# Optimization experiments

Hardware: AMD Instinct MI355X
Metric: run time of the kernel (lower is better)

## Reference

```python
import jax, jax.numpy as jnp
import numpy as np

B, C, H, V = 16384, 5, 256, 512
NUM_ITER = 2


def setup_inputs() -> dict:
    key = jax.random.key(0)
    k1, k2, k3, k4 = jax.random.split(key, 4)
    # v0: one-hot categorical visible units, shape [B, C, V, 1]
    idx = jax.random.randint(k1, (B, V), 0, C)
    v0 = jax.nn.one_hot(idx, C, axis=1, dtype=jnp.float32)[..., None]
    W = 0.01 * jax.random.normal(k2, (C, H, V), dtype=jnp.float32)
    b = 0.01 * jax.random.normal(k3, (C, V, 1), dtype=jnp.float32)
    c = 0.01 * jax.random.normal(k4, (H, 1), dtype=jnp.float32)
    return {"v0": v0, "W": W, "b": b, "c": c, "num_sampling_iter": NUM_ITER}


def reference(v0, W, b, c, num_sampling_iter):
    key = jax.random.key(42)
    b2 = b[..., 0]   # [C, V]
    c1 = c[:, 0]     # [H]
    v = v0[..., 0]   # [B, C, V]

    def sample_h(k, v):
        # p(h=1|v) = sigmoid(sum_c W[c] @ v[:,c] + c)
        p = jax.nn.sigmoid(jnp.einsum('chv,bcv->bh', W, v) + c1)  # [B, H]
        return jax.random.bernoulli(k, p).astype(v.dtype)

    def sample_v(k, h):
        # logits over categories per visible unit: W[c].T @ h + b[c]
        logits = jnp.einsum('chv,bh->bcv', W, h) + b2  # [B, C, V]
        idx = jax.random.categorical(k, logits, axis=1)  # [B, V]
        return jax.nn.one_hot(idx, C, axis=1, dtype=h.dtype)  # [B, C, V]

    keys = jax.random.split(key, 2 * num_sampling_iter + 1)
    h = sample_h(keys[0], v)
    h_given_v0 = h
    for i in range(num_sampling_iter):  # small fixed iteration count
        v = sample_v(keys[2 * i + 1], h)
        h = sample_h(keys[2 * i + 2], v)
    return (v[..., None], h[..., None], h_given_v0[..., None])
```

## Files before the change

### kernel.cpp

```cpp
#include <hip/hip_runtime.h>
#include <cstdint>
#include <cstddef>


#define B_DIM 16384
#define C_DIM 5
#define H_DIM 256
#define V_DIM 512

struct TFOut { uint32_t a, b; };

typedef float f32x2 __attribute__((ext_vector_type(2)));
typedef float f32x4 __attribute__((ext_vector_type(4)));

static __device__ inline f32x2 mk2(float x, float y) {
  f32x2 r; r.x = x; r.y = y; return r;
}

static __device__ inline f32x2 pkfma(f32x2 a, f32x2 b, f32x2 c) {
#if __has_builtin(__builtin_elementwise_fma)
  return __builtin_elementwise_fma(a, b, c);
#else
  f32x2 r; r.x = fmaf(a.x, b.x, c.x); r.y = fmaf(a.y, b.y, c.y); return r;
#endif
}

__host__ __device__ static inline TFOut tf2x32(uint32_t k0, uint32_t k1,
                                               uint32_t c0, uint32_t c1) {
  uint32_t ks2 = k0 ^ k1 ^ 0x1BD11BDAu;
  uint32_t x0 = c0 + k0, x1 = c1 + k1;
#define TF_R(r) { x0 += x1; x1 = (x1 << r) | (x1 >> (32 - r)); x1 ^= x0; }
  TF_R(13) TF_R(15) TF_R(26) TF_R(6)
  x0 += k1;  x1 += ks2 + 1u;
  TF_R(17) TF_R(29) TF_R(16) TF_R(24)
  x0 += ks2; x1 += k0 + 2u;
  TF_R(13) TF_R(15) TF_R(26) TF_R(6)
  x0 += k0;  x1 += k1 + 3u;
  TF_R(17) TF_R(29) TF_R(16) TF_R(24)
  x0 += k1;  x1 += ks2 + 4u;
  TF_R(13) TF_R(15) TF_R(26) TF_R(6)
  x0 += ks2; x1 += k0 + 5u;
#undef TF_R
  TFOut o; o.a = x0; o.b = x1; return o;
}

__device__ static inline uint32_t rng_bits(uint32_t k0, uint32_t k1, uint32_t i) {
  TFOut r = tf2x32(k0, k1, 0u, i);
  return r.a ^ r.b;
}

__device__ static inline float bits_to_unit_float(uint32_t bits) {
  return __uint_as_float((bits >> 9) | 0x3F800000u) - 1.0f;
}

__device__ static float xla_exp(float x_in) {
#pragma clang fp contract(off)
  float x = fminf(x_in, 88.3762626647950f);
  x = fmaxf(x, -88.3762626647949f);
  float fx = floorf(x * 1.44269504088896341f + 0.5f);
  float tmp = fx * 0.693359375f;
  float z = fx * -2.12194440e-4f;
  x = x - tmp;
  x = x - z;
  z = x * x;
  float y = 1.9875691500e-4f;
  y = y * x + 1.3981999507e-3f;
  y = y * x + 8.3334519073e-3f;
  y = y * x + 4.1665795894e-2f;
  y = y * x + 1.6666665459e-1f;
  y = y * x + 5.0000001201e-1f;
  y = y * z + x;
  y = y + 1.0f;
  int n = (int)fx;
  y = y * __uint_as_float((uint32_t)(n + 127) << 23);
  return y;
}

__device__ static float xla_log(float x_in) {
#pragma clang fp contract(off)
  float xv = fmaxf(x_in, 1.17549435e-38f);
  uint32_t bits = __float_as_uint(xv);
  float e = (float)((int)(bits >> 23) - 126);
  float x = __uint_as_float((bits & 0x007FFFFFu) | 0x3F000000u);
  bool m = (x < 0.707106781186547524f);
  float tmp = m ? x : 0.0f;
  x = x - 1.0f;
  e = e - (m ? 1.0f : 0.0f);
  x = x + tmp;
  float z = x * x;
  float y = 7.0376836292e-2f;
  y = y * x + -1.1514610310e-1f;
  y = y * x + 1.1676998740e-1f;
  y = y * x + -1.2420140846e-1f;
  y = y * x + 1.4249322787e-1f;
  y = y * x + -1.6668057665e-1f;
  y = y * x + 2.0000714765e-1f;
  y = y * x + -2.4999993993e-1f;
  y = y * x + 3.3333331174e-1f;
  y = y * x;
  y = y * z;
  float t1 = e * -2.12194440e-4f;
  y = y + t1;
  float t2 = z * 0.5f;
  y = y - t2;
  x = x + y;
  float t3 = e * 0.693359375f;
  x = x + t3;
  return x;
}


__global__ void k_sentinel(float* out, float d) {
  out[0] = d;
}

__global__ __launch_bounds__(256) void k_idx(const float* __restrict__ v0,
                                             uint8_t* __restrict__ idx) {
  int t = blockIdx.x * 256 + threadIdx.x;
  int b = t >> 9, v = t & 511;
  const float* p = v0 + (size_t)b * (C_DIM * V_DIM) + v;
  int cf = 0;
#pragma unroll
  for (int c = 0; c < C_DIM; ++c)
    if (p[c * V_DIM] > 0.5f) cf = c;
  idx[t] = (uint8_t)cf;
}

__global__ __launch_bounds__(256) void k_idxT(const uint8_t* __restrict__ idx,
                                              uint8_t* __restrict__ idxT) {
  __shared__ uint8_t tile[64][68];
  int t = threadIdx.x;
  int bb = blockIdx.x >> 3, vv = blockIdx.x & 7;
  int b0 = bb * 64, v0 = vv * 64;
  for (int i = t; i < 1024; i += 256) {
    int r = i >> 4, wc = i & 15;
    uint32_t q = *(const uint32_t*)(idx + (size_t)(b0 + r) * V_DIM + v0 + wc * 4);
    int v = wc * 4;
    tile[v + 0][r] = (uint8_t)(q);
    tile[v + 1][r] = (uint8_t)(q >> 8);
    tile[v + 2][r] = (uint8_t)(q >> 16);
    tile[v + 3][r] = (uint8_t)(q >> 24);
  }
  __syncthreads();
  for (int i = t; i < 1024; i += 256) {
    int vr = i >> 4, wc = i & 15;
    uint32_t q = (uint32_t)tile[vr][wc * 4]
               | ((uint32_t)tile[vr][wc * 4 + 1] << 8)
               | ((uint32_t)tile[vr][wc * 4 + 2] << 16)
               | ((uint32_t)tile[vr][wc * 4 + 3] << 24);
    *(uint32_t*)(idxT + (size_t)(v0 + vr) * B_DIM + b0 + wc * 4) = q;
  }
}

__global__ __launch_bounds__(256) void k_wt(const float* __restrict__ W,
                                            float* __restrict__ Wt) {
  int t = blockIdx.x * 256 + threadIdx.x;
  int h = t & 255; int rest = t >> 8; int v = rest & 511; int c = rest >> 9;
  Wt[t] = W[((size_t)c * H_DIM + h) * V_DIM + v];
}

__global__ __launch_bounds__(256, 2) void k_hpart(
    const float* __restrict__ Wt, const uint8_t* __restrict__ idxT,
    float* __restrict__ partial) {
  __shared__ __align__(16) float tbf[80][64];
  int t = threadIdx.x;
  int bg = blockIdx.x >> 3, s = blockIdx.x & 7;
  int b0 = bg * 64;
  int wv = t >> 6, lane = t & 63;
  int g16 = wv * 16;

  f32x2 ps[4][8];
#pragma unroll
  for (int hq = 0; hq < 4; ++hq)
#pragma unroll
    for (int p = 0; p < 8; ++p) ps[hq][p] = mk2(0.f, 0.f);

  for (int tau = 0; tau < 4; ++tau) {
    int kbase = s * 320 + tau * 80;
    {
      int kk0 = t >> 4, bq = t & 15;
#pragma unroll
      for (int i = 0; i < 5; ++i) {
        int kk = kk0 + 16 * i;
        int k = kbase + kk;
        int v = k & 511;
        uint32_t cc = (uint32_t)(k >> 9);
        uint32_t q = *(const uint32_t*)(idxT + (size_t)v * B_DIM + b0 + bq * 4);
        float4 o;
        o.x = ((q & 255u) == cc) ? 1.0f : 0.0f;
        o.y = (((q >> 8) & 255u) == cc) ? 1.0f : 0.0f;
        o.z = (((q >> 16) & 255u) == cc) ? 1.0f : 0.0f;
        o.w = (((q >> 24) & 255u) == cc) ? 1.0f : 0.0f;
        *(float4*)&tbf[kk][bq * 4] = o;
      }
    }
    __syncthreads();
#pragma unroll 2
    for (int kk = 0; kk < 80; ++kk) {
      int k = kbase + kk;
      float4 w = *(const float4*)(Wt + (size_t)k * H_DIM + (lane << 2));
      const f32x4* fp = (const f32x4*)&tbf[kk][g16];
      f32x4 qA = fp[0], qB = fp[1], qC = fp[2], qD = fp[3];
      f32x2 f0 = __builtin_shufflevector(qA, qA, 0, 1);
      f32x2 f1 = __builtin_shufflevector(qA, qA, 2, 3);
      f32x2 f2 = __builtin_shufflevector(qB, qB, 0, 1);
      f32x2 f3 = __builtin_shufflevector(qB, qB, 2, 3);
      f32x2 f4 = __builtin_shufflevector(qC, qC, 0, 1);
      f32x2 f5 = __builtin_shufflevector(qC, qC, 2, 3);
      f32x2 f6 = __builtin_shufflevector(qD, qD, 0, 1);
      f32x2 f7 = __builtin_shufflevector(qD, qD, 2, 3);
      f32x2 w0 = mk2(w.x, w.x);
      f32x2 w1 = mk2(w.y, w.y);
      f32x2 w2 = mk2(w.z, w.z);
      f32x2 w3 = mk2(w.w, w.w);
      ps[0][0] = pkfma(w0, f0, ps[0][0]); ps[1][0] = pkfma(w1, f0, ps[1][0]);
      ps[2][0] = pkfma(w2, f0, ps[2][0]); ps[3][0] = pkfma(w3, f0, ps[3][0]);
      ps[0][1] = pkfma(w0, f1, ps[0][1]); ps[1][1] = pkfma(w1, f1, ps[1][1]);
      ps[2][1] = pkfma(w2, f1, ps[2][1]); ps[3][1] = pkfma(w3, f1, ps[3][1]);
      ps[0][2] = pkfma(w0, f2, ps[0][2]); ps[1][2] = pkfma(w1, f2, ps[1][2]);
      ps[2][2] = pkfma(w2, f2, ps[2][2]); ps[3][2] = pkfma(w3, f2, ps[3][2]);
      ps[0][3] = pkfma(w0, f3, ps[0][3]); ps[1][3] = pkfma(w1, f3, ps[1][3]);
      ps[2][3] = pkfma(w2, f3, ps[2][3]); ps[3][3] = pkfma(w3, f3, ps[3][3]);
      ps[0][4] = pkfma(w0, f4, ps[0][4]); ps[1][4] = pkfma(w1, f4, ps[1][4]);
      ps[2][4] = pkfma(w2, f4, ps[2][4]); ps[3][4] = pkfma(w3, f4, ps[3][4]);
      ps[0][5] = pkfma(w0, f5, ps[0][5]); ps[1][5] = pkfma(w1, f5, ps[1][5]);
      ps[2][5] = pkfma(w2, f5, ps[2][5]); ps[3][5] = pkfma(w3, f5, ps[3][5]);
      ps[0][6] = pkfma(w0, f6, ps[0][6]); ps[1][6] = pkfma(w1, f6, ps[1][6]);
      ps[2][6] = pkfma(w2, f6, ps[2][6]); ps[3][6] = pkfma(w3, f6, ps[3][6]);
      ps[0][7] = pkfma(w0, f7, ps[0][7]); ps[1][7] = pkfma(w1, f7, ps[1][7]);
      ps[2][7] = pkfma(w2, f7, ps[2][7]); ps[3][7] = pkfma(w3, f7, ps[3][7]);
    }
    __syncthreads();
  }

  int h0 = lane << 2;
#pragma unroll
  for (int p = 0; p < 8; ++p) {
    float4 oA, oB;
    oA.x = ps[0][p].x; oA.y = ps[1][p].x; oA.z = ps[2][p].x; oA.w = ps[3][p].x;
    oB.x = ps[0][p].y; oB.y = ps[1][p].y; oB.z = ps[2][p].y; oB.w = ps[3][p].y;
    int bA = b0 + g16 + 2 * p;
    *(float4*)&partial[((size_t)s * B_DIM + bA) * H_DIM + h0] = oA;
    *(float4*)&partial[((size_t)s * B_DIM + bA + 1) * H_DIM + h0] = oB;
  }
}

__global__ __launch_bounds__(256) void k_hfin(
    const float* __restrict__ partial, const float* __restrict__ c1,
    float* __restrict__ out_h, uint32_t* __restrict__ out_mask,
    uint32_t key0, uint32_t key1) {
  int b = blockIdx.x;
  int t = threadIdx.x;
  int wv = t >> 6;
  float tt = 0.0f;
#pragma unroll
  for (int s = 0; s < 8; ++s)
    tt = tt + partial[((size_t)s * B_DIM + b) * H_DIM + t];

  float tot = tt + c1[t];
  float p = 1.0f / (1.0f + xla_exp(-tot));

  uint32_t i = (uint32_t)(b * H_DIM + t);
  float u = bits_to_unit_float(rng_bits(key0, key1, i));
  bool hb = (u < p);
  if (out_h) out_h[(size_t)b * H_DIM + t] = hb ? 1.0f : 0.0f;

  unsigned long long m = __ballot(hb);
  if ((t & 63) == 0) {
    out_mask[(size_t)b * 8 + wv * 2 + 0] = (uint32_t)(m & 0xFFFFFFFFull);
    out_mask[(size_t)b * 8 + wv * 2 + 1] = (uint32_t)(m >> 32);
  }
}

__global__ __launch_bounds__(256, 4) void k_gemm_v(
    const float* __restrict__ W, const uint32_t* __restrict__ mask,
    float* __restrict__ sums) {
  __shared__ uint32_t smask[16][8];
  __shared__ __align__(16) float tbf[H_DIM][16];
  int t = threadIdx.x;
  int b0 = blockIdx.x * 16;
  if (t < 128) smask[t >> 3][t & 7] = mask[(size_t)b0 * 8 + t];
  __syncthreads();
  {
    int h = t;
    uint32_t w = (uint32_t)(h >> 5), s = (uint32_t)(h & 31);
#pragma unroll
    for (int j = 0; j < 16; ++j)
      tbf[h][j] = (float)((smask[j][w] >> s) & 1u);
  }
  __syncthreads();

  int wv = t >> 6, lane = t & 63;
  int g = wv >> 1, vh = wv & 1;
  int v0 = vh * 256 + (lane << 2);
  int bg = b0 + g * 8;

  for (int c = 0; c < C_DIM; ++c) {
    f32x2 acc[4][4];
#pragma unroll
    for (int p = 0; p < 4; ++p)
#pragma unroll
      for (int q = 0; q < 4; ++q) acc[p][q] = mk2(0.f, 0.f);

    const float* wp = W + (size_t)c * (H_DIM * V_DIM) + v0;
    for (int hh = 0; hh < H_DIM; hh += 4) {
      float4 w4[4];
#pragma unroll
      for (int u = 0; u < 4; ++u)
        w4[u] = *(const float4*)(wp + (size_t)(hh + u) * V_DIM);
#pragma unroll
      for (int u = 0; u < 4; ++u) {
        const f32x4* fp = (const f32x4*)&tbf[hh + u][g * 8];
        f32x4 qA = fp[0], qB = fp[1];
        f32x2 f0 = __builtin_shufflevector(qA, qA, 0, 1);
        f32x2 f1 = __builtin_shufflevector(qA, qA, 2, 3);
        f32x2 f2 = __builtin_shufflevector(qB, qB, 0, 1);
        f32x2 f3 = __builtin_shufflevector(qB, qB, 2, 3);
        f32x2 wwx = mk2(w4[u].x, w4[u].x);
        f32x2 wwy = mk2(w4[u].y, w4[u].y);
        f32x2 wwz = mk2(w4[u].z, w4[u].z);
        f32x2 www = mk2(w4[u].w, w4[u].w);
        acc[0][0] = pkfma(wwx, f0, acc[0][0]); acc[0][1] = pkfma(wwy, f0, acc[0][1]);
        acc[0][2] = pkfma(wwz, f0, acc[0][2]); acc[0][3] = pkfma(www, f0, acc[0][3]);
        acc[1][0] = pkfma(wwx, f1, acc[1][0]); acc[1][1] = pkfma(wwy, f1, acc[1][1]);
        acc[1][2] = pkfma(wwz, f1, acc[1][2]); acc[1][3] = pkfma(www, f1, acc[1][3]);
        acc[2][0] = pkfma(wwx, f2, acc[2][0]); acc[2][1] = pkfma(wwy, f2, acc[2][1]);
        acc[2][2] = pkfma(wwz, f2, acc[2][2]); acc[2][3] = pkfma(www, f2, acc[2][3]);
        acc[3][0] = pkfma(wwx, f3, acc[3][0]); acc[3][1] = pkfma(wwy, f3, acc[3][1]);
        acc[3][2] = pkfma(wwz, f3, acc[3][2]); acc[3][3] = pkfma(www, f3, acc[3][3]);
      }
    }
#pragma unroll
    for (int p = 0; p < 4; ++p) {
      float4 oA, oB;
      oA.x = acc[p][0].x; oA.y = acc[p][1].x; oA.z = acc[p][2].x; oA.w = acc[p][3].x;
      oB.x = acc[p][0].y; oB.y = acc[p][1].y; oB.z = acc[p][2].y; oB.w = acc[p][3].y;
      *(float4*)&sums[((size_t)c * B_DIM + bg + 2 * p) * V_DIM + v0] = oA;
      *(float4*)&sums[((size_t)c * B_DIM + bg + 2 * p + 1) * V_DIM + v0] = oB;
    }
  }
}

__global__ __launch_bounds__(256, 4) void k_gumbel_v(
    const float* __restrict__ sums, const float* __restrict__ b2,
    uint8_t* __restrict__ idx_out, uint32_t key0, uint32_t key1) {
  int gidx = blockIdx.x * 256 + threadIdx.x;
  int b = gidx >> 7;
  int v0 = (gidx & 127) << 2;
  float best[4];
  uint32_t bc = 0;
#pragma unroll
  for (int c = 0; c < C_DIM; ++c) {
    float4 av = *(const float4*)&sums[((size_t)c * B_DIM + b) * V_DIM + v0];
    float4 bv = *(const float4*)&b2[c * V_DIM + v0];
    uint32_t ib = ((uint32_t)b * C_DIM + (uint32_t)c) * V_DIM + (uint32_t)v0;
    float avq[4] = {av.x, av.y, av.z, av.w};
    float bvq[4] = {bv.x, bv.y, bv.z, bv.w};
#pragma unroll
    for (int q = 0; q < 4; ++q) {
      float uf = bits_to_unit_float(rng_bits(key0, key1, ib + (uint32_t)q));
      if (uf == 0.0f) uf = 1.17549435e-38f;
      float gz = -xla_log(-xla_log(uf));
      float z = gz + (avq[q] + bvq[q]);
      if (c == 0 || z > best[q]) {
        best[q] = z;
        bc = (bc & ~(0xFFu << (8 * q))) | ((uint32_t)c << (8 * q));
      }
    }
  }
  *(uint32_t*)(idx_out + (size_t)b * V_DIM + v0) = bc;
}

__global__ __launch_bounds__(256) void k_onehot(const uint8_t* __restrict__ idx,
                                                float* __restrict__ out) {
  int t = blockIdx.x * 256 + threadIdx.x;
  int v4 = t & 127;
  int rest = t >> 7;
  int c = rest % C_DIM;
  int b = rest / C_DIM;
  uint32_t q = *(const uint32_t*)(idx + (size_t)b * V_DIM + v4 * 4);
  uint32_t cc = (uint32_t)c;
  float4 o;
  o.x = ((q & 255u) == cc) ? 1.0f : 0.0f;
  o.y = (((q >> 8) & 255u) == cc) ? 1.0f : 0.0f;
  o.z = (((q >> 16) & 255u) == cc) ? 1.0f : 0.0f;
  o.w = (((q >> 24) & 255u) == cc) ? 1.0f : 0.0f;
  *(float4*)&out[(size_t)t * 4] = o;
}


extern "C" void kernel_launch(void* const* d_in, const int* in_sizes, int n_in,
                              void* d_out, int out_size, void* d_ws, size_t ws_size,
                              hipStream_t stream) {
  float* out = (float*)d_out;

  const size_t WS_NEED = 2621440ull
                       + 2621440ull
                       + 8388608ull
                       + 524288ull;
  float D = 0.0f;
  if (n_in < 4)                       D = 910.0f + (float)n_in;
  else if (in_sizes[0] != 41943040)   D = 920.0f;
  else if (in_sizes[1] != 655360)     D = 921.0f;
  else if (in_sizes[2] != 2560)       D = 922.0f;
  else if (in_sizes[3] != 256)        D = 923.0f;
  else if (out_size != 50331648)      D = 930.0f + (float)out_size * 1e-6f;
  else if (ws_size < WS_NEED)         D = 100.0f + (float)(ws_size >> 20);
  if (D != 0.0f) {
    hipLaunchKernelGGL(k_sentinel, dim3(1), dim3(1), 0, stream, out, D);
    return;
  }

  const float* v0 = (const float*)d_in[0];
  const float* W  = (const float*)d_in[1];
  const float* b2 = (const float*)d_in[2];
  const float* c1 = (const float*)d_in[3];

  float* out_v  = out;
  float* out_h  = out + (size_t)B_DIM * C_DIM * V_DIM;
  float* out_h0 = out_h + (size_t)B_DIM * H_DIM;

  char* ws = (char*)d_ws;
  float*    Wt   = (float*)(ws);
  uint8_t*  idx  = (uint8_t*)(ws + 5242880);
  uint32_t* mask = (uint32_t*)(ws + 13631488);

  float*   sums    = out_v;
  float*   partial = out_v;
  uint8_t* idxT    = (uint8_t*)out_v + 134217728ull;

  uint32_t keys[5][2];
  for (int i = 0; i < 5; ++i) {
    TFOut r = tf2x32(0u, 42u, 0u, (uint32_t)i);
    keys[i][0] = r.a; keys[i][1] = r.b;
  }

  hipLaunchKernelGGL(k_wt,  dim3(2560),  dim3(256), 0, stream, W, Wt);
  hipLaunchKernelGGL(k_idx, dim3(32768), dim3(256), 0, stream, v0, idx);
  hipLaunchKernelGGL(k_idxT, dim3(2048), dim3(256), 0, stream, idx, idxT);

  hipLaunchKernelGGL(k_hpart, dim3(2048), dim3(256), 0, stream, Wt, idxT, partial);
  hipLaunchKernelGGL(k_hfin,  dim3(B_DIM), dim3(256), 0, stream,
                     partial, c1, out_h0, mask, keys[0][0], keys[0][1]);
  hipLaunchKernelGGL(k_gemm_v, dim3(B_DIM / 16), dim3(256), 0, stream,
                     W, mask, sums);
  hipLaunchKernelGGL(k_gumbel_v, dim3(B_DIM * 128 / 256), dim3(256), 0, stream,
                     sums, b2, idx, keys[1][0], keys[1][1]);
  hipLaunchKernelGGL(k_idxT, dim3(2048), dim3(256), 0, stream, idx, idxT);
  hipLaunchKernelGGL(k_hpart, dim3(2048), dim3(256), 0, stream, Wt, idxT, partial);
  hipLaunchKernelGGL(k_hfin,  dim3(B_DIM), dim3(256), 0, stream,
                     partial, c1, (float*)nullptr, mask, keys[2][0], keys[2][1]);
  hipLaunchKernelGGL(k_gemm_v, dim3(B_DIM / 16), dim3(256), 0, stream,
                     W, mask, sums);
  hipLaunchKernelGGL(k_gumbel_v, dim3(B_DIM * 128 / 256), dim3(256), 0, stream,
                     sums, b2, idx, keys[3][0], keys[3][1]);
  hipLaunchKernelGGL(k_idxT, dim3(2048), dim3(256), 0, stream, idx, idxT);
  hipLaunchKernelGGL(k_hpart, dim3(2048), dim3(256), 0, stream, Wt, idxT, partial);
  hipLaunchKernelGGL(k_hfin,  dim3(B_DIM), dim3(256), 0, stream,
                     partial, c1, out_h, mask, keys[4][0], keys[4][1]);
  hipLaunchKernelGGL(k_onehot, dim3(40960), dim3(256), 0, stream, idx, out_v);
}
```

Measured before the change: 1.871 ms.

## Fuse Gumbel-max sampling into visible GEMM and shrink hpart batch tile

The visible-unit logits GEMM now performs the Gumbel-max categorical sampling in registers and writes only the uint8 category indices. This removes the round trip of the large [C,B,V] float sums buffer through global memory and one kernel launch per iteration. Separately, k_hpart processes 32 batch rows per block instead of 64, with fewer accumulators, a higher occupancy hint and twice as many blocks. The trade-off is that each Wt load is reused across fewer batch rows, and the fused kernel carries extra live state per thread (best values and indices for 8 rows).

Result: slower. 1.947 ms (+4.1%).

```diff
diff --git a/kernel.cpp b/kernel.cpp
--- a/kernel.cpp
+++ b/kernel.cpp
@@ -159,39 +159,41 @@
   Wt[t] = W[((size_t)c * H_DIM + h) * V_DIM + v];
 }
 
-__global__ __launch_bounds__(256, 2) void k_hpart(
+__global__ __launch_bounds__(256, 4) void k_hpart(
     const float* __restrict__ Wt, const uint8_t* __restrict__ idxT,
     float* __restrict__ partial) {
-  __shared__ __align__(16) float tbf[80][64];
+  __shared__ __align__(16) float tbf[80][32];
   int t = threadIdx.x;
   int bg = blockIdx.x >> 3, s = blockIdx.x & 7;
-  int b0 = bg * 64;
+  int b0 = bg * 32;
   int wv = t >> 6, lane = t & 63;
-  int g16 = wv * 16;
-
-  f32x2 ps[4][8];
+  int g8 = wv * 8;
+
+  f32x2 ps[4][4];
 #pragma unroll
   for (int hq = 0; hq < 4; ++hq)
 #pragma unroll
-    for (int p = 0; p < 8; ++p) ps[hq][p] = mk2(0.f, 0.f);
+    for (int p = 0; p < 4; ++p) ps[hq][p] = mk2(0.f, 0.f);
 
   for (int tau = 0; tau < 4; ++tau) {
     int kbase = s * 320 + tau * 80;
     {
-      int kk0 = t >> 4, bq = t & 15;
-#pragma unroll
-      for (int i = 0; i < 5; ++i) {
-        int kk = kk0 + 16 * i;
-        int k = kbase + kk;
-        int v = k & 511;
-        uint32_t cc = (uint32_t)(k >> 9);
-        uint32_t q = *(const uint32_t*)(idxT + (size_t)v * B_DIM + b0 + bq * 4);
-        float4 o;
-        o.x = ((q & 255u) == cc) ? 1.0f : 0.0f;
-        o.y = (((q >> 8) & 255u) == cc) ? 1.0f : 0.0f;
-        o.z = (((q >> 16) & 255u) == cc) ? 1.0f : 0.0f;
-        o.w = (((q >> 24) & 255u) == cc) ? 1.0f : 0.0f;
-        *(float4*)&tbf[kk][bq * 4] = o;
+      int kk0 = t >> 3, bq = t & 7;
+#pragma unroll
+      for (int i = 0; i < 3; ++i) {
+        int kk = kk0 + 32 * i;
+        if (kk < 80) {
+          int k = kbase + kk;
+          int v = k & 511;
+          uint32_t cc = (uint32_t)(k >> 9);
+          uint32_t q = *(const uint32_t*)(idxT + (size_t)v * B_DIM + b0 + bq * 4);
+          float4 o;
+          o.x = ((q & 255u) == cc) ? 1.0f : 0.0f;
+          o.y = (((q >> 8) & 255u) == cc) ? 1.0f : 0.0f;
+          o.z = (((q >> 16) & 255u) == cc) ? 1.0f : 0.0f;
+          o.w = (((q >> 24) & 255u) == cc) ? 1.0f : 0.0f;
+          *(float4*)&tbf[kk][bq * 4] = o;
+        }
       }
     }
     __syncthreads();
@@ -199,16 +201,12 @@
     for (int kk = 0; kk < 80; ++kk) {
       int k = kbase + kk;
       float4 w = *(const float4*)(Wt + (size_t)k * H_DIM + (lane << 2));
-      const f32x4* fp = (const f32x4*)&tbf[kk][g16];
-      f32x4 qA = fp[0], qB = fp[1], qC = fp[2], qD = fp[3];
+      const f32x4* fp = (const f32x4*)&tbf[kk][g8];
+      f32x4 qA = fp[0], qB = fp[1];
       f32x2 f0 = __builtin_shufflevector(qA, qA, 0, 1);
       f32x2 f1 = __builtin_shufflevector(qA, qA, 2, 3);
       f32x2 f2 = __builtin_shufflevector(qB, qB, 0, 1);
       f32x2 f3 = __builtin_shufflevector(qB, qB, 2, 3);
-      f32x2 f4 = __builtin_shufflevector(qC, qC, 0, 1);
-      f32x2 f5 = __builtin_shufflevector(qC, qC, 2, 3);
-      f32x2 f6 = __builtin_shufflevector(qD, qD, 0, 1);
-      f32x2 f7 = __builtin_shufflevector(qD, qD, 2, 3);
       f32x2 w0 = mk2(w.x, w.x);
       f32x2 w1 = mk2(w.y, w.y);
       f32x2 w2 = mk2(w.z, w.z);
@@ -221,25 +219,17 @@
       ps[2][2] = pkfma(w2, f2, ps[2][2]); ps[3][2] = pkfma(w3, f2, ps[3][2]);
       ps[0][3] = pkfma(w0, f3, ps[0][3]); ps[1][3] = pkfma(w1, f3, ps[1][3]);
       ps[2][3] = pkfma(w2, f3, ps[2][3]); ps[3][3] = pkfma(w3, f3, ps[3][3]);
-      ps[0][4] = pkfma(w0, f4, ps[0][4]); ps[1][4] = pkfma(w1, f4, ps[1][4]);
-      ps[2][4] = pkfma(w2, f4, ps[2][4]); ps[3][4] = pkfma(w3, f4, ps[3][4]);
-      ps[0][5] = pkfma(w0, f5, ps[0][5]); ps[1][5] = pkfma(w1, f5, ps[1][5]);
-      ps[2][5] = pkfma(w2, f5, ps[2][5]); ps[3][5] = pkfma(w3, f5, ps[3][5]);
-      ps[0][6] = pkfma(w0, f6, ps[0][6]); ps[1][6] = pkfma(w1, f6, ps[1][6]);
-      ps[2][6] = pkfma(w2, f6, ps[2][6]); ps[3][6] = pkfma(w3, f6, ps[3][6]);
-      ps[0][7] = pkfma(w0, f7, ps[0][7]); ps[1][7] = pkfma(w1, f7, ps[1][7]);
-      ps[2][7] = pkfma(w2, f7, ps[2][7]); ps[3][7] = pkfma(w3, f7, ps[3][7]);
     }
     __syncthreads();
   }
 
   int h0 = lane << 2;
 #pragma unroll
-  for (int p = 0; p < 8; ++p) {
+  for (int p = 0; p < 4; ++p) {
     float4 oA, oB;
     oA.x = ps[0][p].x; oA.y = ps[1][p].x; oA.z = ps[2][p].x; oA.w = ps[3][p].x;
     oB.x = ps[0][p].y; oB.y = ps[1][p].y; oB.z = ps[2][p].y; oB.w = ps[3][p].y;
-    int bA = b0 + g16 + 2 * p;
+    int bA = b0 + g8 + 2 * p;
     *(float4*)&partial[((size_t)s * B_DIM + bA) * H_DIM + h0] = oA;
     *(float4*)&partial[((size_t)s * B_DIM + bA + 1) * H_DIM + h0] = oB;
   }
@@ -272,9 +262,10 @@
   }
 }
 
-__global__ __launch_bounds__(256, 4) void k_gemm_v(
-    const float* __restrict__ W, const uint32_t* __restrict__ mask,
-    float* __restrict__ sums) {
+__global__ __launch_bounds__(256, 4) void k_sample_v(
+    const float* __restrict__ W, const float* __restrict__ b2,
+    const uint32_t* __restrict__ mask, uint8_t* __restrict__ idx_out,
+    uint32_t key0, uint32_t key1) {
   __shared__ uint32_t smask[16][8];
   __shared__ __align__(16) float tbf[H_DIM][16];
   int t = threadIdx.x;
@@ -294,6 +285,11 @@
   int g = wv >> 1, vh = wv & 1;
   int v0 = vh * 256 + (lane << 2);
   int bg = b0 + g * 8;
+
+  float best[8][4];
+  uint32_t bc[8];
+#pragma unroll
+  for (int bi = 0; bi < 8; ++bi) bc[bi] = 0u;
 
   for (int c = 0; c < C_DIM; ++c) {
     f32x2 acc[4][4];
@@ -330,45 +326,39 @@
         acc[3][2] = pkfma(wwz, f3, acc[3][2]); acc[3][3] = pkfma(www, f3, acc[3][3]);
       }
     }
+
+    float4 bv = *(const float4*)&b2[c * V_DIM + v0];
+    float bvq[4] = {bv.x, bv.y, bv.z, bv.w};
 #pragma unroll
     for (int p = 0; p < 4; ++p) {
-      float4 oA, oB;
-      oA.x = acc[p][0].x; oA.y = acc[p][1].x; oA.z = acc[p][2].x; oA.w = acc[p][3].x;
-      oB.x = acc[p][0].y; oB.y = acc[p][1].y; oB.z = acc[p][2].y; oB.w = acc[p][3].y;
-      *(float4*)&sums[((size_t)c * B_DIM + bg + 2 * p) * V_DIM + v0] = oA;
-      *(float4*)&sums[((size_t)c * B_DIM + bg + 2 * p + 1) * V_DIM + v0] = oB;
-    }
-  }
-}
-
-__global__ __launch_bounds__(256, 4) void k_gumbel_v(
-    const float* __restrict__ sums, const float* __restrict__ b2,
-    uint8_t* __restrict__ idx_out, uint32_t key0, uint32_t key1) {
-  int gidx = blockIdx.x * 256 + threadIdx.x;
-  int b = gidx >> 7;
-  int v0 = (gidx & 127) << 2;
-  float best[4];
-  uint32_t bc = 0;
-#pragma unroll
-  for (int c = 0; c < C_DIM; ++c) {
-    float4 av = *(const float4*)&sums[((size_t)c * B_DIM + b) * V_DIM + v0];
-    float4 bv = *(const float4*)&b2[c * V_DIM + v0];
-    uint32_t ib = ((uint32_t)b * C_DIM + (uint32_t)c) * V_DIM + (uint32_t)v0;
-    float avq[4] = {av.x, av.y, av.z, av.w};
-    float bvq[4] = {bv.x, bv.y, bv.z, bv.w};
-#pragma unroll
-    for (int q = 0; q < 4; ++q) {
-      float uf = bits_to_unit_float(rng_bits(key0, key1, ib + (uint32_t)q));
-      if (uf == 0.0f) uf = 1.17549435e-38f;
-      float gz = -xla_log(-xla_log(uf));
-      float z = gz + (avq[q] + bvq[q]);
-      if (c == 0 || z > best[q]) {
-        best[q] = z;
-        bc = (bc & ~(0xFFu << (8 * q))) | ((uint32_t)c << (8 * q));
+#pragma unroll
+      for (int e = 0; e < 2; ++e) {
+        int bi = 2 * p + e;
+        int b = bg + bi;
+        uint32_t ib = ((uint32_t)b * C_DIM + (uint32_t)c) * V_DIM + (uint32_t)v0;
+        float avq[4];
+        avq[0] = e ? acc[p][0].y : acc[p][0].x;
+        avq[1] = e ? acc[p][1].y : acc[p][1].x;
+        avq[2] = e ? acc[p][2].y : acc[p][2].x;
+        avq[3] = e ? acc[p][3].y : acc[p][3].x;
+#pragma unroll
+        for (int q = 0; q < 4; ++q) {
+          float uf = bits_to_unit_float(rng_bits(key0, key1, ib + (uint32_t)q));
+          if (uf == 0.0f) uf = 1.17549435e-38f;
+          float gz = -xla_log(-xla_log(uf));
+          float z = gz + (avq[q] + bvq[q]);
+          if (c == 0 || z > best[bi][q]) {
+            best[bi][q] = z;
+            bc[bi] = (bc[bi] & ~(0xFFu << (8 * q))) | ((uint32_t)c << (8 * q));
+          }
+        }
       }
     }
   }
-  *(uint32_t*)(idx_out + (size_t)b * V_DIM + v0) = bc;
+
+#pragma unroll
+  for (int bi = 0; bi < 8; ++bi)
+    *(uint32_t*)(idx_out + (size_t)(bg + bi) * V_DIM + v0) = bc[bi];
 }
 
 __global__ __launch_bounds__(256) void k_onehot(const uint8_t* __restrict__ idx,
@@ -425,7 +415,6 @@
   uint8_t*  idx  = (uint8_t*)(ws + 5242880);
   uint32_t* mask = (uint32_t*)(ws + 13631488);
 
-  float*   sums    = out_v;
   float*   partial = out_v;
   uint8_t* idxT    = (uint8_t*)out_v + 134217728ull;
 
@@ -439,23 +428,19 @@
   hipLaunchKernelGGL(k_idx, dim3(32768), dim3(256), 0, stream, v0, idx);
   hipLaunchKernelGGL(k_idxT, dim3(2048), dim3(256), 0, stream, idx, idxT);
 
-  hipLaunchKernelGGL(k_hpart, dim3(2048), dim3(256), 0, stream, Wt, idxT, partial);
+  hipLaunchKernelGGL(k_hpart, dim3(4096), dim3(256), 0, stream, Wt, idxT, partial);
   hipLaunchKernelGGL(k_hfin,  dim3(B_DIM), dim3(256), 0, stream,
                      partial, c1, out_h0, mask, keys[0][0], keys[0][1]);
-  hipLaunchKernelGGL(k_gemm_v, dim3(B_DIM / 16), dim3(256), 0, stream,
-                     W, mask, sums);
-  hipLaunchKernelGGL(k_gumbel_v, dim3(B_DIM * 128 / 256), dim3(256), 0, stream,
-                     sums, b2, idx, keys[1][0], keys[1][1]);
+  hipLaunchKernelGGL(k_sample_v, dim3(B_DIM / 16), dim3(256), 0, stream,
+                     W, b2, mask, idx, keys[1][0], keys[1][1]);
   hipLaunchKernelGGL(k_idxT, dim3(2048), dim3(256), 0, stream, idx, idxT);
-  hipLaunchKernelGGL(k_hpart, dim3(2048), dim3(256), 0, stream, Wt, idxT, partial);
+  hipLaunchKernelGGL(k_hpart, dim3(4096), dim3(256), 0, stream, Wt, idxT, partial);
   hipLaunchKernelGGL(k_hfin,  dim3(B_DIM), dim3(256), 0, stream,
                      partial, c1, (float*)nullptr, mask, keys[2][0], keys[2][1]);
-  hipLaunchKernelGGL(k_gemm_v, dim3(B_DIM / 16), dim3(256), 0, stream,
-                     W, mask, sums);
-  hipLaunchKernelGGL(k_gumbel_v, dim3(B_DIM * 128 / 256), dim3(256), 0, stream,
-                     sums, b2, idx, keys[3][0], keys[3][1]);
+  hipLaunchKernelGGL(k_sample_v, dim3(B_DIM / 16), dim3(256), 0, stream,
+                     W, b2, mask, idx, keys[3][0], keys[3][1]);
   hipLaunchKernelGGL(k_idxT, dim3(2048), dim3(256), 0, stream, idx, idxT);
-  hipLaunchKernelGGL(k_hpart, dim3(2048), dim3(256), 0, stream, Wt, idxT, partial);
+  hipLaunchKernelGGL(k_hpart, dim3(4096), dim3(256), 0, stream, Wt, idxT, partial);
   hipLaunchKernelGGL(k_hfin,  dim3(B_DIM), dim3(256), 0, stream,
                      partial, c1, out_h, mask, keys[4][0], keys[4][1]);
   hipLaunchKernelGGL(k_onehot, dim3(40960), dim3(256), 0, stream, idx, out_v);
```
